# Kernel optimization log

Hardware: AMD Instinct MI355X
Metric: run time of the kernel (lower is better)

Reference implementation:

```python
import jax, jax.numpy as jnp
import numpy as np

N_HEADS = 16
D_MODEL = 1024
D_HEAD = D_MODEL // N_HEADS  # 64


def setup_inputs() -> dict:
    key = jax.random.key(0)
    ks = jax.random.split(key, 7)
    B, S = 16, 1024
    x = jax.random.normal(ks[0], (B, S, D_MODEL), dtype=jnp.float32)
    # Per-head torch Linear params: weight [out, in] = [D_HEAD, D_HEAD], bias [D_HEAD].
    # Xavier-uniform scale for square weight: sqrt(6/(fan_in+fan_out)).
    lim = float(np.sqrt(6.0 / (D_HEAD + D_HEAD)))
    blim = float(1.0 / np.sqrt(D_HEAD))  # torch default bias init U(-1/sqrt(fan_in), ...)
    Wq = jax.random.uniform(ks[1], (N_HEADS, D_HEAD, D_HEAD), jnp.float32, -lim, lim)
    Wk = jax.random.uniform(ks[2], (N_HEADS, D_HEAD, D_HEAD), jnp.float32, -lim, lim)
    Wv = jax.random.uniform(ks[3], (N_HEADS, D_HEAD, D_HEAD), jnp.float32, -lim, lim)
    bq = jax.random.uniform(ks[4], (N_HEADS, D_HEAD), jnp.float32, -blim, blim)
    bk = jax.random.uniform(ks[5], (N_HEADS, D_HEAD), jnp.float32, -blim, blim)
    bv = jax.random.uniform(ks[6], (N_HEADS, D_HEAD), jnp.float32, -blim, blim)
    return {"sequences": x, "Wq": Wq, "Wk": Wk, "Wv": Wv, "bq": bq, "bk": bk, "bv": bv}


def reference(sequences, Wq, Wk, Wv, bq, bk, bv):
    B, S, D = sequences.shape
    H, dh = N_HEADS, D_HEAD
    # Split feature dim into heads: [B, S, H, dh] (same chunks the torch loop slices).
    x = sequences.reshape(B, S, H, dh)
    # torch Linear: y = x @ W.T + b  -> einsum over the 'in' axis of W[out, in].
    q = jnp.einsum("bshd,hed->bshe", x, Wq) + bq  # [B,S,H,dh]
    k = jnp.einsum("bshd,hed->bshe", x, Wk) + bk
    v = jnp.einsum("bshd,hed->bshe", x, Wv) + bv
    scale = 1.0 / jnp.sqrt(jnp.asarray(dh, dtype=sequences.dtype))
    scores = jnp.einsum("bshe,bthe->bhst", q, k) * scale  # [B,H,S,S]
    weights = jax.nn.softmax(scores, axis=-1)
    attended = jnp.einsum("bhst,bthe->bshe", weights, v)  # [B,S,H,dh]
    # hstack over heads == concat along feature dim.
    return attended.reshape(B, S, D)
```

## Files before the change

### kernel.cpp

```cpp
#include <hip/hip_runtime.h>

constexpr int B_ = 16, S_ = 1024, H_ = 16, DH_ = 64, DM_ = 1024;

typedef short bf16x8 __attribute__((ext_vector_type(8)));
typedef unsigned short us8 __attribute__((ext_vector_type(8)));
typedef unsigned short us4 __attribute__((ext_vector_type(4)));
typedef float f32x4 __attribute__((ext_vector_type(4)));
typedef float f32x16 __attribute__((ext_vector_type(16)));
typedef unsigned u32x4 __attribute__((ext_vector_type(4)));

__device__ __forceinline__ unsigned short f2b(float f) {
    unsigned u = __builtin_bit_cast(unsigned, f);
    u += 0x7FFFu + ((u >> 16) & 1u);
    return (unsigned short)(u >> 16);
}

__device__ __forceinline__ int swz(int r, int c) { return (r << 6) + (c ^ ((r & 7) << 3)); }

__device__ __forceinline__ unsigned cvtpk(float lo, float hi) {
    unsigned r;
    asm("v_cvt_pk_bf16_f32 %0, %1, %2" : "=v"(r) : "v"(lo), "v"(hi));
    return r;
}
__device__ __forceinline__ void permswap(unsigned& a, unsigned& b) {
    asm volatile("v_permlane32_swap_b32 %0, %1" : "+v"(a), "+v"(b));
}

#define QSCALE 0.18033688011112042f

__global__ __launch_bounds__(256) void proj_kernel(
    const float* __restrict__ x,
    const float* __restrict__ wq, const float* __restrict__ wk, const float* __restrict__ wv,
    const float* __restrict__ bq, const float* __restrict__ bk, const float* __restrict__ bv,
    unsigned short* __restrict__ qo, unsigned short* __restrict__ ko,
    unsigned short* __restrict__ vto)
{
    __shared__ unsigned short xs[128 * 64];
    __shared__ unsigned short wls[3][64 * 64];

    const int tid = threadIdx.x;
    const int bid = blockIdx.x;
    const int chunk = bid & 7, bh = bid >> 3;
    const int b = bh >> 4, h = bh & 15;
    const int s0 = chunk * 128;
    const int lane = tid & 63, w = tid >> 6;
    const int lr = lane & 15, lg = lane >> 4;

    #pragma unroll
    for (int it = 0; it < 4; ++it) {
        int item = it * 256 + tid;
        int row = item >> 3, c = (item & 7) << 3;
        const float* src = x + (size_t)(b * S_ + s0 + row) * DM_ + h * DH_ + c;
        float4 f0 = *(const float4*)src;
        float4 f1 = *(const float4*)(src + 4);
        us8 v = { f2b(f0.x), f2b(f0.y), f2b(f0.z), f2b(f0.w),
                  f2b(f1.x), f2b(f1.y), f2b(f1.z), f2b(f1.w) };
        *(us8*)&xs[swz(row, c)] = v;
    }
    const float* wsrc[3] = { wq, wk, wv };
    #pragma unroll
    for (int mtx = 0; mtx < 3; ++mtx) {
        const float scl = (mtx == 0) ? QSCALE : 1.0f;
        #pragma unroll
        for (int it = 0; it < 2; ++it) {
            int item = it * 256 + tid;
            int row = item >> 3, c = (item & 7) << 3;
            const float* src = wsrc[mtx] + (size_t)h * 4096 + row * 64 + c;
            float4 f0 = *(const float4*)src;
            float4 f1 = *(const float4*)(src + 4);
            us8 v = { f2b(f0.x * scl), f2b(f0.y * scl), f2b(f0.z * scl), f2b(f0.w * scl),
                      f2b(f1.x * scl), f2b(f1.y * scl), f2b(f1.z * scl), f2b(f1.w * scl) };
            *(us8*)&wls[mtx][swz(row, c)] = v;
        }
    }
    __syncthreads();

    bf16x8 af[2][2];
    #pragma unroll
    for (int mt = 0; mt < 2; ++mt)
        #pragma unroll
        for (int k2 = 0; k2 < 2; ++k2)
            af[mt][k2] = *(const bf16x8*)&xs[swz(w * 32 + mt * 16 + lr, k2 * 32 + lg * 8)];

    const float* bias[3] = { bq, bk, bv };
    #pragma unroll
    for (int mtx = 0; mtx < 3; ++mtx) {
        const float bscl = (mtx == 0) ? QSCALE : 1.0f;
        #pragma unroll
        for (int mt = 0; mt < 2; ++mt) {
            #pragma unroll
            for (int n4 = 0; n4 < 4; ++n4) {
                f32x4 acc = { 0.f, 0.f, 0.f, 0.f };
                #pragma unroll
                for (int k2 = 0; k2 < 2; ++k2) {
                    bf16x8 bf_ = *(const bf16x8*)&wls[mtx][swz(n4 * 16 + lr, k2 * 32 + lg * 8)];
                    acc = __builtin_amdgcn_mfma_f32_16x16x32_bf16(af[mt][k2], bf_, acc, 0, 0, 0);
                }
                const int e = n4 * 16 + lr;
                const float bb = bias[mtx][h * DH_ + e] * bscl;
                const int srow0 = s0 + w * 32 + mt * 16 + lg * 4;
                if (mtx == 0) {
                    #pragma unroll
                    for (int r = 0; r < 4; ++r)
                        qo[(size_t)(bh * S_ + srow0 + r) * 64 + e] = f2b(acc[r] + bb);
                } else if (mtx == 1) {
                    #pragma unroll
                    for (int r = 0; r < 4; ++r)
                        ko[(size_t)(bh * S_ + srow0 + r) * 64 + e] = f2b(acc[r] + bb);
                } else {
                    us4 pk = { f2b(acc[0] + bb), f2b(acc[1] + bb),
                               f2b(acc[2] + bb), f2b(acc[3] + bb) };
                    *(us4*)&vto[(size_t)(bh * 64 + e) * S_ + srow0] = pk;
                }
            }
        }
    }
}

__global__ __launch_bounds__(256) void attn_kernel(
    const unsigned short* __restrict__ qw, const unsigned short* __restrict__ kw,
    const unsigned short* __restrict__ vtw, float* __restrict__ out)
{
    __shared__ unsigned short ks[2][64 * 64];
    __shared__ unsigned short vs[2][64 * 64];

    const int tid = threadIdx.x, lane = tid & 63, w = tid >> 6;
    int bid = blockIdx.x;
    bid = (bid & 7) * 256 + (bid >> 3);
    const int qt = bid & 7, bh = bid >> 3;
    const int b = bh >> 4, h = bh & 15;
    const int q0 = qt * 128;
    const int l31 = lane & 31, hi = lane >> 5, hi8 = hi << 3;

    const unsigned short* kbase = kw + (size_t)bh * S_ * 64;
    const unsigned short* vbase = vtw + (size_t)bh * 64 * S_;

    bf16x8 qf[4];
    {
        const unsigned short* qp = qw + (size_t)(bh * S_ + q0 + w * 32 + l31) * 64 + hi8;
        #pragma unroll
        for (int s = 0; s < 4; ++s) qf[s] = *(const bf16x8*)(qp + s * 16);
    }

    const int srow = tid >> 3, sc = (tid & 7) << 3;
    const int swzA = swz(srow, sc), swzB = swz(srow + 32, sc);

    f32x16 o0, o1, zro;
    #pragma unroll
    for (int i = 0; i < 16; ++i) { o0[i] = 0.f; o1[i] = 0.f; zro[i] = 0.f; }
    float lreg = 0.f;

    us8 sk0 = *(const us8*)(kbase + (size_t)srow * 64 + sc);
    us8 sk1 = *(const us8*)(kbase + (size_t)(srow + 32) * 64 + sc);
    us8 sv0 = *(const us8*)(vbase + (size_t)srow * S_ + sc);
    us8 sv1 = *(const us8*)(vbase + (size_t)(srow + 32) * S_ + sc);
    *(us8*)&ks[0][swzA] = sk0;  *(us8*)&ks[0][swzB] = sk1;
    *(us8*)&vs[0][swzA] = sv0;  *(us8*)&vs[0][swzB] = sv1;
    __syncthreads();

    constexpr int NT = S_ / 64;
    for (int t = 0; t < NT; ++t) {
        const int cur = t & 1;

        if (t + 1 < NT) {
            const int n1 = (t + 1) * 64;
            sk0 = *(const us8*)(kbase + (size_t)(n1 + srow) * 64 + sc);
            sk1 = *(const us8*)(kbase + (size_t)(n1 + srow + 32) * 64 + sc);
            sv0 = *(const us8*)(vbase + (size_t)srow * S_ + n1 + sc);
            sv1 = *(const us8*)(vbase + (size_t)(srow + 32) * S_ + n1 + sc);
        }

        f32x16 p0, p1;
        {
            bf16x8 ka0 = *(const bf16x8*)&ks[cur][swz(l31,      hi8)];
            bf16x8 ka1 = *(const bf16x8*)&ks[cur][swz(32 + l31, hi8)];
            p0 = __builtin_amdgcn_mfma_f32_32x32x16_bf16(ka0, qf[0], zro, 0, 0, 0);
            p1 = __builtin_amdgcn_mfma_f32_32x32x16_bf16(ka1, qf[0], zro, 0, 0, 0);
        }
        #pragma unroll
        for (int s = 1; s < 4; ++s) {
            bf16x8 ka0 = *(const bf16x8*)&ks[cur][swz(l31,      s * 16 + hi8)];
            bf16x8 ka1 = *(const bf16x8*)&ks[cur][swz(32 + l31, s * 16 + hi8)];
            p0 = __builtin_amdgcn_mfma_f32_32x32x16_bf16(ka0, qf[s], p0, 0, 0, 0);
            p1 = __builtin_amdgcn_mfma_f32_32x32x16_bf16(ka1, qf[s], p1, 0, 0, 0);
        }

        #pragma unroll
        for (int i = 0; i < 16; ++i) {
            p0[i] = __builtin_amdgcn_exp2f(p0[i]);
            p1[i] = __builtin_amdgcn_exp2f(p1[i]);
        }
        float rs = 0.f;
        #pragma unroll
        for (int i = 0; i < 16; ++i) rs += p0[i] + p1[i];
        rs += __shfl_xor(rs, 32);
        lreg += rs;

        bf16x8 pa[4];
        {
            unsigned a0 = cvtpk(p0[0], p0[1]),  b0 = cvtpk(p0[4], p0[5]);
            unsigned a1 = cvtpk(p0[2], p0[3]),  b1 = cvtpk(p0[6], p0[7]);
            permswap(a0, b0); permswap(a1, b1);
            u32x4 t0 = { a0, a1, b0, b1 };
            pa[0] = __builtin_bit_cast(bf16x8, t0);
            unsigned a2 = cvtpk(p0[8], p0[9]),   b2 = cvtpk(p0[12], p0[13]);
            unsigned a3 = cvtpk(p0[10], p0[11]), b3 = cvtpk(p0[14], p0[15]);
            permswap(a2, b2); permswap(a3, b3);
            u32x4 t1 = { a2, a3, b2, b3 };
            pa[1] = __builtin_bit_cast(bf16x8, t1);
            unsigned a4 = cvtpk(p1[0], p1[1]),  b4 = cvtpk(p1[4], p1[5]);
            unsigned a5 = cvtpk(p1[2], p1[3]),  b5 = cvtpk(p1[6], p1[7]);
            permswap(a4, b4); permswap(a5, b5);
            u32x4 t2 = { a4, a5, b4, b5 };
            pa[2] = __builtin_bit_cast(bf16x8, t2);
            unsigned a6 = cvtpk(p1[8], p1[9]),   b6 = cvtpk(p1[12], p1[13]);
            unsigned a7 = cvtpk(p1[10], p1[11]), b7 = cvtpk(p1[14], p1[15]);
            permswap(a6, b6); permswap(a7, b7);
            u32x4 t3 = { a6, a7, b6, b7 };
            pa[3] = __builtin_bit_cast(bf16x8, t3);
        }

        #pragma unroll
        for (int s = 0; s < 4; ++s) {
            bf16x8 vb0 = *(const bf16x8*)&vs[cur][swz(l31,      s * 16 + hi8)];
            bf16x8 vb1 = *(const bf16x8*)&vs[cur][swz(32 + l31, s * 16 + hi8)];
            o0 = __builtin_amdgcn_mfma_f32_32x32x16_bf16(pa[s], vb0, o0, 0, 0, 0);
            o1 = __builtin_amdgcn_mfma_f32_32x32x16_bf16(pa[s], vb1, o1, 0, 0, 0);
        }

        if (t + 1 < NT) {
            const int nb = cur ^ 1;
            *(us8*)&ks[nb][swzA] = sk0;  *(us8*)&ks[nb][swzB] = sk1;
            *(us8*)&vs[nb][swzA] = sv0;  *(us8*)&vs[nb][swzB] = sv1;
        }
        __syncthreads();
    }

    const float linv = 1.0f / lreg;
    #pragma unroll
    for (int r = 0; r < 16; ++r) {
        const int q = (r & 3) + 8 * (r >> 2) + (hi << 2);
        const float iv = __shfl(linv, q);
        float* op = out + (size_t)(b * S_ + q0 + w * 32 + q) * DM_ + h * DH_ + l31;
        op[0]  = o0[r] * iv;
        op[32] = o1[r] * iv;
    }
}

extern "C" void kernel_launch(void* const* d_in, const int* in_sizes, int n_in,
                              void* d_out, int out_size, void* d_ws, size_t ws_size,
                              hipStream_t stream) {
    const float* x  = (const float*)d_in[0];
    const float* wq = (const float*)d_in[1];
    const float* wk = (const float*)d_in[2];
    const float* wv = (const float*)d_in[3];
    const float* bq = (const float*)d_in[4];
    const float* bk = (const float*)d_in[5];
    const float* bv = (const float*)d_in[6];
    float* out = (float*)d_out;

    const size_t per = (size_t)B_ * H_ * S_ * DH_;
    unsigned short* qws  = (unsigned short*)d_ws;
    unsigned short* kws  = qws + per;
    unsigned short* vtws = kws + per;

    proj_kernel<<<dim3(2048), dim3(256), 0, stream>>>(x, wq, wk, wv, bq, bk, bv,
                                                      qws, kws, vtws);
    attn_kernel<<<dim3(2048), dim3(256), 0, stream>>>(qws, kws, vtws, out);
}
```

Measured before the change: 132.3 us.

## Use direct global-to-LDS loads for K/V tiles and halve attention block size

Replaces the register-staged K/V tile loads (global load into VGPRs, then LDS store) with global_load_lds direct-to-LDS transfers, applying the XOR swizzle on the source column instead. Attention blocks shrink to 128 threads covering 64 query rows, so the grid doubles to 4096 blocks. The intent is to cut VGPR pressure and LDS store instructions and to raise occupancy, but each block now reloads the full K/V for fewer queries, which doubles K/V traffic. The trailing barrier is dropped on the last iteration.

```diff
diff --git a/kernel.cpp b/kernel.cpp
--- a/kernel.cpp
+++ b/kernel.cpp
@@ -24,6 +24,12 @@
 }
 __device__ __forceinline__ void permswap(unsigned& a, unsigned& b) {
     asm volatile("v_permlane32_swap_b32 %0, %1" : "+v"(a), "+v"(b));
+}
+
+__device__ __forceinline__ void gload16(const unsigned short* g, unsigned short* l) {
+    __builtin_amdgcn_global_load_lds(
+        (const __attribute__((address_space(1))) void*)g,
+        (__attribute__((address_space(3))) void*)l, 16, 0, 0);
 }
 
 #define QSCALE 0.18033688011112042f
@@ -117,7 +123,7 @@
     }
 }
 
-__global__ __launch_bounds__(256) void attn_kernel(
+__global__ __launch_bounds__(128) void attn_kernel(
     const unsigned short* __restrict__ qw, const unsigned short* __restrict__ kw,
     const unsigned short* __restrict__ vtw, float* __restrict__ out)
 {
@@ -126,14 +132,17 @@
 
     const int tid = threadIdx.x, lane = tid & 63, w = tid >> 6;
     int bid = blockIdx.x;
-    bid = (bid & 7) * 256 + (bid >> 3);
-    const int qt = bid & 7, bh = bid >> 3;
+    bid = (bid & 7) * 512 + (bid >> 3);
+    const int qt = bid & 15, bh = bid >> 4;
     const int b = bh >> 4, h = bh & 15;
-    const int q0 = qt * 128;
+    const int q0 = qt * 64;
     const int l31 = lane & 31, hi = lane >> 5, hi8 = hi << 3;
 
     const unsigned short* kbase = kw + (size_t)bh * S_ * 64;
     const unsigned short* vbase = vtw + (size_t)bh * 64 * S_;
+
+    const int srow8 = lane >> 3;
+    const int colsw = ((lane & 7) ^ (lane >> 3)) << 3;
 
     bf16x8 qf[4];
     {
@@ -142,20 +151,17 @@
         for (int s = 0; s < 4; ++s) qf[s] = *(const bf16x8*)(qp + s * 16);
     }
 
-    const int srow = tid >> 3, sc = (tid & 7) << 3;
-    const int swzA = swz(srow, sc), swzB = swz(srow + 32, sc);
-
     f32x16 o0, o1, zro;
     #pragma unroll
     for (int i = 0; i < 16; ++i) { o0[i] = 0.f; o1[i] = 0.f; zro[i] = 0.f; }
     float lreg = 0.f;
 
-    us8 sk0 = *(const us8*)(kbase + (size_t)srow * 64 + sc);
-    us8 sk1 = *(const us8*)(kbase + (size_t)(srow + 32) * 64 + sc);
-    us8 sv0 = *(const us8*)(vbase + (size_t)srow * S_ + sc);
-    us8 sv1 = *(const us8*)(vbase + (size_t)(srow + 32) * S_ + sc);
-    *(us8*)&ks[0][swzA] = sk0;  *(us8*)&ks[0][swzB] = sk1;
-    *(us8*)&vs[0][swzA] = sv0;  *(us8*)&vs[0][swzB] = sv1;
+    #pragma unroll
+    for (int i = 0; i < 4; ++i) {
+        const int br = w * 32 + i * 8;
+        gload16(kbase + (size_t)(br + srow8) * 64 + colsw, &ks[0][br * 64]);
+        gload16(vbase + (size_t)(br + srow8) * S_ + colsw, &vs[0][br * 64]);
+    }
     __syncthreads();
 
     constexpr int NT = S_ / 64;
@@ -164,10 +170,13 @@
 
         if (t + 1 < NT) {
             const int n1 = (t + 1) * 64;
-            sk0 = *(const us8*)(kbase + (size_t)(n1 + srow) * 64 + sc);
-            sk1 = *(const us8*)(kbase + (size_t)(n1 + srow + 32) * 64 + sc);
-            sv0 = *(const us8*)(vbase + (size_t)srow * S_ + n1 + sc);
-            sv1 = *(const us8*)(vbase + (size_t)(srow + 32) * S_ + n1 + sc);
+            const int nb = cur ^ 1;
+            #pragma unroll
+            for (int i = 0; i < 4; ++i) {
+                const int br = w * 32 + i * 8;
+                gload16(kbase + (size_t)(n1 + br + srow8) * 64 + colsw, &ks[nb][br * 64]);
+                gload16(vbase + (size_t)(br + srow8) * S_ + n1 + colsw, &vs[nb][br * 64]);
+            }
         }
 
         f32x16 p0, p1;
@@ -228,12 +237,7 @@
             o1 = __builtin_amdgcn_mfma_f32_32x32x16_bf16(pa[s], vb1, o1, 0, 0, 0);
         }
 
-        if (t + 1 < NT) {
-            const int nb = cur ^ 1;
-            *(us8*)&ks[nb][swzA] = sk0;  *(us8*)&ks[nb][swzB] = sk1;
-            *(us8*)&vs[nb][swzA] = sv0;  *(us8*)&vs[nb][swzB] = sv1;
-        }
-        __syncthreads();
+        if (t + 1 < NT) __syncthreads();
     }
 
     const float linv = 1.0f / lreg;
@@ -266,5 +270,5 @@
 
     proj_kernel<<<dim3(2048), dim3(256), 0, stream>>>(x, wq, wk, wv, bq, bk, bv,
                                                       qws, kws, vtws);
-    attn_kernel<<<dim3(2048), dim3(256), 0, stream>>>(qws, kws, vtws, out);
-}
+    attn_kernel<<<dim3(4096), dim3(128), 0, stream>>>(qws, kws, vtws, out);
+}
```

New measurement: 159.1 us. +20.3%, slower.
